# Optimization experiments

Hardware: AMD Instinct MI355X
Metric: run time of the kernel (lower is better)

The kernel has to match this reference:

```python
import jax, jax.numpy as jnp
import numpy as np

VOCAB, S, D, H, DH, L, W1S, DFF = 50265, 4096, 768, 12, 64, 2, 256, 3072


def layer_norm(x, g, b, eps=1e-5):
    m = jnp.mean(x, axis=-1, keepdims=True)
    v = jnp.mean((x - m) ** 2, axis=-1, keepdims=True)
    return (x - m) * jax.lax.rsqrt(v + eps) * g + b


def sliding_global_attn(q, k, v, att, w=W1S):
    # q,k,v: [B,H,S,Dh]; att: [B,S] float (1 real / 0 pad). Longformer-style
    # sliding window (one-sided w) + global attention on token 0.
    B, nh, S_, Dh = q.shape
    nc = S_ // w
    q = q * (Dh ** -0.5)
    k_pad = jnp.pad(k, ((0, 0), (0, 0), (w, w), (0, 0)))
    v_pad = jnp.pad(v, ((0, 0), (0, 0), (w, w), (0, 0)))
    idx = jnp.arange(nc)[:, None] * w + jnp.arange(3 * w)[None, :]  # [nc,3w] into padded axis
    k_band = k_pad[:, :, idx]  # [B,H,nc,3w,Dh]
    v_band = v_pad[:, :, idx]
    qc = q.reshape(B, nh, nc, w, Dh)
    s_loc = jnp.einsum('bhcqd,bhckd->bhcqk', qc, k_band)  # [B,H,nc,w,3w]
    rel = jnp.arange(3 * w)[None, :] - jnp.arange(w)[:, None]  # [w,3w]
    band_ok = (rel >= 0) & (rel <= 2 * w)
    key_abs = idx - w  # [nc,3w] absolute key positions
    in_seq = (key_abs >= 0) & (key_abs < S_) & (key_abs != 0)  # token 0 handled by global column
    key_real = att[:, jnp.clip(key_abs, 0, S_ - 1)] > 0  # [B,nc,3w]
    valid = band_ok[None, None, None] & in_seq[None, None, :, None, :] & key_real[:, None, :, None, :]
    s_loc = jnp.where(valid, s_loc, -1e9)
    s_g = jnp.einsum('bhcqd,bhd->bhcq', qc, k[:, :, 0])  # global key column
    p = jax.nn.softmax(jnp.concatenate([s_g[..., None], s_loc], axis=-1), axis=-1)
    out = (jnp.einsum('bhcq,bhd->bhcqd', p[..., 0], v[:, :, 0])
           + jnp.einsum('bhcqk,bhckd->bhcqd', p[..., 1:], v_band)).reshape(B, nh, S_, Dh)
    # global token 0 attends to everything
    s0 = jnp.where(att[:, None, :] > 0, jnp.einsum('bhd,bhsd->bhs', q[:, :, 0], k), -1e9)
    out0 = jnp.einsum('bhs,bhsd->bhd', jax.nn.softmax(s0, axis=-1), v)
    return out.at[:, :, 0].set(out0)


def setup_inputs() -> dict:
    key = jax.random.key(0)
    ks = jax.random.split(key, 16)
    sc = 0.02
    inp = {
        'input_ids': jax.random.randint(ks[0], (2, S), 0, VOCAB, dtype=jnp.int64)
        if jax.config.jax_enable_x64 else jax.random.randint(ks[0], (2, S), 0, VOCAB, dtype=jnp.int32),
        'attention_mask': jnp.ones((2, S), dtype=jnp.int32),
        'word_emb': sc * jax.random.normal(ks[1], (VOCAB, D), jnp.float32),
        'pos_emb': sc * jax.random.normal(ks[2], (S, D), jnp.float32),
        'emb_ln_g': jnp.ones((D,), jnp.float32), 'emb_ln_b': jnp.zeros((D,), jnp.float32),
        'Wq': sc * jax.random.normal(ks[3], (L, D, D), jnp.float32), 'bq': jnp.zeros((L, D), jnp.float32),
        'Wk': sc * jax.random.normal(ks[4], (L, D, D), jnp.float32), 'bk': jnp.zeros((L, D), jnp.float32),
        'Wv': sc * jax.random.normal(ks[5], (L, D, D), jnp.float32), 'bv': jnp.zeros((L, D), jnp.float32),
        'Wo': sc * jax.random.normal(ks[6], (L, D, D), jnp.float32), 'bo': jnp.zeros((L, D), jnp.float32),
        'ln1_g': jnp.ones((L, D), jnp.float32), 'ln1_b': jnp.zeros((L, D), jnp.float32),
        'Wf1': sc * jax.random.normal(ks[7], (L, D, DFF), jnp.float32), 'bf1': jnp.zeros((L, DFF), jnp.float32),
        'Wf2': sc * jax.random.normal(ks[8], (L, DFF, D), jnp.float32), 'bf2': jnp.zeros((L, D), jnp.float32),
        'ln2_g': jnp.ones((L, D), jnp.float32), 'ln2_b': jnp.zeros((L, D), jnp.float32),
        'Wh1': sc * jax.random.normal(ks[9], (D, 256), jnp.float32), 'bh1': jnp.zeros((256,), jnp.float32),
        'Wh2': sc * jax.random.normal(ks[10], (256, 14), jnp.float32), 'bh2': jnp.zeros((14,), jnp.float32),
    }
    return inp


def reference(input_ids, attention_mask, word_emb, pos_emb, emb_ln_g, emb_ln_b,
              Wq, bq, Wk, bk, Wv, bv, Wo, bo, ln1_g, ln1_b,
              Wf1, bf1, Wf2, bf2, ln2_g, ln2_b, Wh1, bh1, Wh2, bh2):
    B, S_ = input_ids.shape
    att = attention_mask.astype(jnp.float32)
    x = word_emb[input_ids] + pos_emb[None, :S_, :]
    x = layer_norm(x, emb_ln_g, emb_ln_b)
    for l in range(L):
        def heads(w, b):
            return (x @ w + b).reshape(B, S_, H, DH).transpose(0, 2, 1, 3)
        q = heads(Wq[l], bq[l]); k = heads(Wk[l], bk[l]); v = heads(Wv[l], bv[l])
        a = sliding_global_attn(q, k, v, att)
        a = a.transpose(0, 2, 1, 3).reshape(B, S_, D) @ Wo[l] + bo[l]
        x = layer_norm(x + a, ln1_g[l], ln1_b[l])
        f = jax.nn.gelu(x @ Wf1[l] + bf1[l]) @ Wf2[l] + bf2[l]
        x = layer_norm(x + f, ln2_g[l], ln2_b[l])
    # masked mean pool
    m = att[..., None]
    pooled = jnp.sum(x * m, axis=1) / jnp.clip(jnp.sum(m, axis=1), 1e-9)
    h = jax.nn.relu(pooled @ Wh1 + bh1)
    return jax.nn.sigmoid(h @ Wh2 + bh2) * 4.0
```

## Files before the change

kernel.cpp:

```cpp
#include <hip/hip_runtime.h>
#include <hip/hip_bf16.h>
#include <math.h>

#define S_LEN 4096
#define D_MODEL 768
#define NHEAD 12
#define DH 64
#define NLAYER 2
#define DFF 3072
#define BATCH 2
#define QSTR 2304

typedef __attribute__((ext_vector_type(8))) __bf16 bf16x8;
typedef __attribute__((ext_vector_type(4))) float f32x4;
typedef __attribute__((ext_vector_type(16))) float f32x16;

__device__ __forceinline__ unsigned short f2bf_bits(float f) {
  unsigned int u = __float_as_uint(f);
  unsigned int r = (u + 0x7fffu + ((u >> 16) & 1u)) >> 16;
  return (unsigned short)r;
}

__device__ __forceinline__ float bf2f(unsigned short u) {
  return __uint_as_float(((unsigned int)u) << 16);
}

__device__ __forceinline__ unsigned int cvtpk_bf16(float lo, float hi) {
  unsigned int d;
  asm("v_cvt_pk_bf16_f32 %0, %1, %2" : "=v"(d) : "v"(lo), "v"(hi));
  return d;
}

__device__ __forceinline__ float gelu_fast(float x) {
  float u = 0.7978845608028654f * (x + 0.044715f * x * x * x);
  float t2 = fminf(fmaxf(2.f * u, -18.f), 18.f);
  float e = __expf(t2);
  return 0.5f * x * (1.f + (e - 1.f) / (e + 1.f));
}

#define ASYNC_COPY16(gsrc, ldst)                                       \
  __builtin_amdgcn_global_load_lds(                                    \
      (const __attribute__((address_space(1))) void*)(gsrc),           \
      (__attribute__((address_space(3))) void*)(ldst), 16, 0, 0)

#define MFMA_BF16(a, b, c) __builtin_amdgcn_mfma_f32_16x16x32_bf16(a, b, c, 0, 0, 0)
#define MFMA32_BF16(a, b, c) __builtin_amdgcn_mfma_f32_32x32x16_bf16(a, b, c, 0, 0, 0)

__device__ __forceinline__ float blk_sum256(float v, float* lds) {
#pragma unroll
  for (int off = 32; off > 0; off >>= 1) v += __shfl_down(v, off, 64);
  __syncthreads();
  if ((threadIdx.x & 63) == 0) lds[threadIdx.x >> 6] = v;
  __syncthreads();
  return lds[0] + lds[1] + lds[2] + lds[3];
}

__global__ __launch_bounds__(256) void wconv_kernel(
    const float* __restrict__ Wq, const float* __restrict__ Wk,
    const float* __restrict__ Wv, const float* __restrict__ Wo,
    const float* __restrict__ Wf1, const float* __restrict__ Wf2,
    unsigned short* __restrict__ Wbf) {
  int id = blockIdx.x;
  const float* src;
  unsigned short* dst;
  int K, N, t;
  if (id < 4608) {
    int m = id / 576;
    t = id % 576;
    int layer = m >> 2, which = m & 3;
    const float* s = (which == 0) ? Wq : (which == 1) ? Wk : (which == 2) ? Wv : Wo;
    src = s + (size_t)layer * 589824;
    dst = Wbf + (size_t)layer * 7077888 + (size_t)which * 589824;
    K = 768; N = 768;
  } else if (id < 9216) {
    int j = id - 4608;
    int layer = j / 2304;
    t = j % 2304;
    src = Wf1 + (size_t)layer * 2359296;
    dst = Wbf + (size_t)layer * 7077888 + 2359296;
    K = 768; N = 3072;
  } else {
    int j = id - 9216;
    int layer = j / 2304;
    t = j % 2304;
    src = Wf2 + (size_t)layer * 2359296;
    dst = Wbf + (size_t)layer * 7077888 + 4718592;
    K = 3072; N = 768;
  }
  int tiles_n = N >> 5;
  int tk = t / tiles_n, tn = t % tiles_n;
  __shared__ float tile[32][33];
  int c = threadIdx.x & 31, r0 = threadIdx.x >> 5;
#pragma unroll
  for (int p = 0; p < 4; ++p) {
    int r = r0 + p * 8;
    tile[r][c] = src[(size_t)(tk * 32 + r) * N + tn * 32 + c];
  }
  __syncthreads();
#pragma unroll
  for (int p = 0; p < 4; ++p) {
    int r = r0 + p * 8;
    dst[(size_t)(tn * 32 + r) * K + tk * 32 + c] = f2bf_bits(tile[c][r]);
  }
}

__global__ __launch_bounds__(256) void embed_ln_kernel(
    const int* __restrict__ ids, const float* __restrict__ wemb,
    const float* __restrict__ pemb, const float* __restrict__ g,
    const float* __restrict__ b, unsigned short* __restrict__ Xb) {
  int row = blockIdx.x;
  int s = row % S_LEN;
  int id = ids[row];
  const float* we = wemb + (size_t)id * D_MODEL;
  const float* pe = pemb + (size_t)s * D_MODEL;
  int t = threadIdx.x;
  __shared__ float lds[4];
  float v0 = we[t] + pe[t];
  float v1 = we[t + 256] + pe[t + 256];
  float v2 = we[t + 512] + pe[t + 512];
  float mean = blk_sum256(v0 + v1 + v2, lds) * (1.f / 768.f);
  float d0 = v0 - mean, d1 = v1 - mean, d2 = v2 - mean;
  float var = blk_sum256(d0 * d0 + d1 * d1 + d2 * d2, lds) * (1.f / 768.f);
  float rs = rsqrtf(var + 1e-5f);
  unsigned short* xb = Xb + (size_t)row * D_MODEL;
  xb[t]       = f2bf_bits(d0 * rs * g[t] + b[t]);
  xb[t + 256] = f2bf_bits(d1 * rs * g[t + 256] + b[t + 256]);
  xb[t + 512] = f2bf_bits(d2 * rs * g[t + 512] + b[t + 512]);
}

__global__ __launch_bounds__(256) void ln_kernel(
    const float* __restrict__ T, const float* __restrict__ g,
    const float* __restrict__ b, unsigned short* __restrict__ Xb) {
  int row = blockIdx.x;
  const float* tp = T + (size_t)row * D_MODEL;
  int t = threadIdx.x;
  __shared__ float lds[4];
  float v0 = tp[t], v1 = tp[t + 256], v2 = tp[t + 512];
  float mean = blk_sum256(v0 + v1 + v2, lds) * (1.f / 768.f);
  float d0 = v0 - mean, d1 = v1 - mean, d2 = v2 - mean;
  float var = blk_sum256(d0 * d0 + d1 * d1 + d2 * d2, lds) * (1.f / 768.f);
  float rs = rsqrtf(var + 1e-5f);
  unsigned short* xb = Xb + (size_t)row * D_MODEL;
  xb[t]       = f2bf_bits(d0 * rs * g[t] + b[t]);
  xb[t + 256] = f2bf_bits(d1 * rs * g[t + 256] + b[t + 256]);
  xb[t + 512] = f2bf_bits(d2 * rs * g[t + 512] + b[t + 512]);
}

template <int MODE>
__global__ __launch_bounds__(256) void gemm32(
    const unsigned short* __restrict__ A, const unsigned short* __restrict__ Bt,
    const float* __restrict__ bias0, const float* __restrict__ bias1,
    const float* __restrict__ bias2, const unsigned short* __restrict__ ResBf,
    void* __restrict__ Cout, int M, int N, int K) {
  __shared__ unsigned short Abuf[3][128 * 32];
  __shared__ unsigned short Bbuf[3][128 * 32];
  const int tid = threadIdx.x;
  const int lane = tid & 63, w = tid >> 6;
  const int wm = w >> 1, wn = w & 1;
  const int l31 = lane & 31, l5 = lane >> 5;

  const int nbx = gridDim.x;
  const int nwg = nbx * gridDim.y;
  const int orig = blockIdx.y * nbx + blockIdx.x;
  const int wgid = (orig & 7) * (nwg >> 3) + (orig >> 3);
  const int m0 = (wgid / nbx) * 128, n0 = (wgid % nbx) * 128;

  f32x16 acc[2][2];
#pragma unroll
  for (int i = 0; i < 2; ++i)
#pragma unroll
    for (int j = 0; j < 2; ++j)
#pragma unroll
      for (int r = 0; r < 16; ++r) acc[i][j][r] = 0.f;

  const int s0 = w * 64 + lane, s1 = s0 + 256;
  const int r0 = s0 >> 2, c0 = (s0 & 3) ^ ((r0 >> 1) & 3);
  const int r1 = s1 >> 2, c1 = (s1 & 3) ^ ((r1 >> 1) & 3);
  const unsigned short* gA0 = A + (size_t)(m0 + r0) * K + c0 * 8;
  const unsigned short* gA1 = A + (size_t)(m0 + r1) * K + c1 * 8;
  const unsigned short* gB0 = Bt + (size_t)(n0 + r0) * K + c0 * 8;
  const unsigned short* gB1 = Bt + (size_t)(n0 + r1) * K + c1 * 8;
  const int dA0 = (w * 64) * 8, dA1 = (256 + w * 64) * 8;

  int aoff[2][2], boff[2][2];
#pragma unroll
  for (int mt = 0; mt < 2; ++mt) {
    int ra = wm * 64 + mt * 32 + l31;
    int rb = wn * 64 + mt * 32 + l31;
    int key_a = (ra >> 1) & 3, key_b = (rb >> 1) & 3;
#pragma unroll
    for (int ks = 0; ks < 2; ++ks) {
      aoff[mt][ks] = ra * 32 + ((((ks << 1) | l5) ^ key_a) << 3);
      boff[mt][ks] = rb * 32 + ((((ks << 1) | l5) ^ key_b) << 3);
    }
  }

#define STAGE(bsel)                                                       \
  {                                                                       \
    ASYNC_COPY16(gA0, &Abuf[bsel][dA0]);                                  \
    ASYNC_COPY16(gA1, &Abuf[bsel][dA1]);                                  \
    ASYNC_COPY16(gB0, &Bbuf[bsel][dA0]);                                  \
    ASYNC_COPY16(gB1, &Bbuf[bsel][dA1]);                                  \
    gA0 += 32; gA1 += 32; gB0 += 32; gB1 += 32;                           \
  }

  const int nk = K >> 5;
  STAGE(0);
  if (nk > 1) STAGE(1);
  asm volatile("s_waitcnt vmcnt(4)" ::: "memory");
  __builtin_amdgcn_s_barrier();
  __builtin_amdgcn_sched_barrier(0);

  int cur = 0;
  for (int kt = 0; kt < nk; ++kt) {
    if (kt + 2 < nk) {
      int nxt = cur + 2;
      if (nxt >= 3) nxt -= 3;
      STAGE(nxt);
    }
    bf16x8 av[2][2], bv[2][2];
#pragma unroll
    for (int mt = 0; mt < 2; ++mt)
#pragma unroll
      for (int ks = 0; ks < 2; ++ks) {
        av[mt][ks] = *(const bf16x8*)(&Abuf[cur][aoff[mt][ks]]);
        bv[mt][ks] = *(const bf16x8*)(&Bbuf[cur][boff[mt][ks]]);
      }
#pragma unroll
    for (int mt = 0; mt < 2; ++mt)
#pragma unroll
      for (int nt = 0; nt < 2; ++nt)
#pragma unroll
        for (int ks = 0; ks < 2; ++ks)
          acc[mt][nt] = MFMA32_BF16(av[mt][ks], bv[nt][ks], acc[mt][nt]);
    if (kt + 1 < nk) {
      if (kt + 2 < nk)
        asm volatile("s_waitcnt vmcnt(4)" ::: "memory");
      else
        asm volatile("s_waitcnt vmcnt(0)" ::: "memory");
      __builtin_amdgcn_s_barrier();
      __builtin_amdgcn_sched_barrier(0);
    }
    cur = (cur == 2) ? 0 : cur + 1;
  }
#undef STAGE

#pragma unroll
  for (int mt = 0; mt < 2; ++mt) {
#pragma unroll
    for (int nt = 0; nt < 2; ++nt) {
      int gc = n0 + wn * 64 + nt * 32 + l31;
      float bsv;
      if (MODE == 4)
        bsv = (gc < 768) ? bias0[gc] : (gc < 1536) ? bias1[gc - 768] : bias2[gc - 1536];
      else
        bsv = bias0[gc];
#pragma unroll
      for (int reg = 0; reg < 16; ++reg) {
        int gr = m0 + wm * 64 + mt * 32 + (reg & 3) + 8 * (reg >> 2) + 4 * l5;
        float v = acc[mt][nt][reg] + bsv;
        if (MODE == 1) v = gelu_fast(v);
        if (MODE == 4 && gc < 768) v *= 0.125f;
        if (MODE == 2) {
          v += bf2f(ResBf[(size_t)gr * 768 + gc]);
          ((float*)Cout)[(size_t)gr * N + gc] = v;
        } else {
          ((unsigned short*)Cout)[(size_t)gr * N + gc] = f2bf_bits(v);
        }
      }
    }
  }
}

__global__ __launch_bounds__(256) void vtrans_kernel(
    const unsigned short* __restrict__ Vsrc, unsigned short* __restrict__ Vt) {
  int kb = blockIdx.x, h = blockIdx.y, b = blockIdx.z;
  int k0 = kb * 64;
  const size_t bs = (size_t)b * S_LEN;
  const size_t bh = (size_t)(b * NHEAD + h);
  __shared__ unsigned short tile[64][72];
  int tid = threadIdx.x;
#pragma unroll
  for (int p = 0; p < 2; ++p) {
    int idx = p * 256 + tid;
    int key = idx >> 3, ch = idx & 7;
    bf16x8 v = *(const bf16x8*)(Vsrc + (bs + k0 + key) * QSTR + h * DH + ch * 8);
    *(bf16x8*)&tile[key][ch * 8] = v;
  }
  __syncthreads();
#pragma unroll
  for (int p = 0; p < 2; ++p) {
    int idx = p * 256 + tid;
    int d = idx >> 3, kc = idx & 7;
    unsigned int w0 = tile[kc * 8 + 0][d] | ((unsigned int)tile[kc * 8 + 1][d] << 16);
    unsigned int w1 = tile[kc * 8 + 2][d] | ((unsigned int)tile[kc * 8 + 3][d] << 16);
    unsigned int w2 = tile[kc * 8 + 4][d] | ((unsigned int)tile[kc * 8 + 5][d] << 16);
    unsigned int w3 = tile[kc * 8 + 6][d] | ((unsigned int)tile[kc * 8 + 7][d] << 16);
    uint4 out = make_uint4(w0, w1, w2, w3);
    *(uint4*)(Vt + (bh * 64 + d) * S_LEN + k0 + kc * 8) = out;
  }
}

__global__ __launch_bounds__(512) void band_attn_kernel(
    const unsigned short* __restrict__ Qg, const unsigned short* __restrict__ Kgb,
    const unsigned short* __restrict__ Vgb, const unsigned short* __restrict__ Vt,
    const int* __restrict__ att, unsigned short* __restrict__ Aout) {
  const int bid = blockIdx.x;
  const int tid = threadIdx.x;
  const int lane = tid & 63, wq = tid >> 6;
  const int g = lane >> 4, cl = lane & 15;

  __shared__ __align__(16) char smem[52224];

  if (bid >= 384) {
    int g2 = bid - 384;
    int h = g2 % NHEAD, b = g2 / NHEAD;
    const size_t bs = (size_t)b * S_LEN;
    float* sc = (float*)smem;
    float* q0 = sc + S_LEN;
    float* red = q0 + 64;
    float* part = red + 8;
    if (tid < 64) q0[tid] = bf2f(Qg[bs * QSTR + h * DH + tid]);
    __syncthreads();
    float lmax = -1e30f;
    for (int s = tid; s < S_LEN; s += 512) {
      const unsigned short* kp = Kgb + (bs + s) * QSTR + h * DH;
      float acc = 0.f;
#pragma unroll
      for (int cc = 0; cc < 8; ++cc) {
        uint4 u = *(const uint4*)(kp + cc * 8);
        const unsigned int* uu = (const unsigned int*)&u;
#pragma unroll
        for (int w2 = 0; w2 < 4; ++w2) {
          unsigned int x = uu[w2];
          acc += q0[cc * 8 + w2 * 2] * __uint_as_float(x << 16);
          acc += q0[cc * 8 + w2 * 2 + 1] * __uint_as_float(x & 0xffff0000u);
        }
      }
      acc = (att[b * S_LEN + s] > 0) ? acc : -1e9f;
      sc[s] = acc;
      lmax = fmaxf(lmax, acc);
    }
#pragma unroll
    for (int off = 32; off > 0; off >>= 1) lmax = fmaxf(lmax, __shfl_down(lmax, off, 64));
    __syncthreads();
    if (lane == 0) red[wq] = lmax;
    __syncthreads();
    float M = red[0];
#pragma unroll
    for (int i = 1; i < 8; ++i) M = fmaxf(M, red[i]);
    float lsum = 0.f;
    for (int s = tid; s < S_LEN; s += 512) {
      float p = __expf(sc[s] - M);
      sc[s] = p;
      lsum += p;
    }
#pragma unroll
    for (int off = 32; off > 0; off >>= 1) lsum += __shfl_down(lsum, off, 64);
    __syncthreads();
    if (lane == 0) red[wq] = lsum;
    __syncthreads();
    float L = red[0];
#pragma unroll
    for (int i = 1; i < 8; ++i) L += red[i];
    int d = tid & 63, chunk = tid >> 6;
    float acc2 = 0.f;
    for (int s = chunk * 512; s < (chunk + 1) * 512; ++s)
      acc2 += sc[s] * bf2f(Vgb[(bs + s) * QSTR + h * DH + d]);
    part[chunk * 64 + d] = acc2;
    __syncthreads();
    if (tid < 64) {
      float v = 0.f;
#pragma unroll
      for (int i = 0; i < 8; ++i) v += part[i * 64 + tid];
      Aout[bs * D_MODEL + h * DH + tid] = f2bf_bits(v / L);
    }
    return;
  }

  const int xcd = bid & 7, within = bid >> 3;
  const int flat = xcd * 48 + within;
  const int c = flat & 15;
  const int hb = flat >> 4;
  const int h = hb % NHEAD, b = hb / NHEAD;
  const size_t bs = (size_t)b * S_LEN;
  const size_t bh = (size_t)(b * NHEAD + h);

  unsigned short* Klds = (unsigned short*)smem;
  unsigned short* Vlds = Klds + 3 * 4096;
  float* kmaskAll = (float*)(Vlds + 3 * 4096);

  const int Q0 = c * 256;

  bf16x8 qf[2][2];
#pragma unroll
  for (int qt = 0; qt < 2; ++qt)
#pragma unroll
    for (int ks = 0; ks < 2; ++ks)
      qf[qt][ks] = *(const bf16x8*)(Qg + (bs + Q0 + wq * 32 + qt * 16 + cl) * QSTR +
                                    h * DH + ks * 32 + g * 8);

  float mrun[2], lrun[2];
  f32x4 oacc[2][4];
#pragma unroll
  for (int qt = 0; qt < 2; ++qt) {
    float sg = 0.f;
#pragma unroll
    for (int ks = 0; ks < 2; ++ks) {
      bf16x8 k0 = *(const bf16x8*)(Kgb + bs * QSTR + h * DH + ks * 32 + g * 8);
#pragma unroll
      for (int j = 0; j < 8; ++j) sg += (float)qf[qt][ks][j] * (float)k0[j];
    }
    sg += __shfl_xor(sg, 16, 64);
    sg += __shfl_xor(sg, 32, 64);
    mrun[qt] = sg;
    lrun[qt] = 1.f;
  }
#pragma unroll
  for (int dt = 0; dt < 4; ++dt) {
    float v0d = bf2f(Vgb[bs * QSTR + h * DH + dt * 16 + cl]);
    f32x4 vv = {v0d, v0d, v0d, v0d};
    oacc[0][dt] = vv;
    oacc[1][dt] = vv;
  }
  for (int i = tid; i < 768; i += 512) {
    int ka = Q0 - 256 + i;
    kmaskAll[i] = (ka >= 1 && ka < S_LEN && att[b * S_LEN + ka] > 0) ? 0.f : -1e9f;
  }
  __syncthreads();

  const int jlo = wq * 32, jhi = wq * 32 + 543;
  const int tlo = (Q0 < 256) ? 4 : 0;
  int thi = (S_LEN + 256 - Q0) >> 6;
  if (thi > 12) thi = 12;

  const int skey = tid >> 3, sch = tid & 7;
  const int srcswzK = (sch ^ (skey & 7)) * 8;

  auto STAGE_T = [&](int t) {
    int p = t % 3;
    int kb0 = Q0 - 256 + t * 64;
    const unsigned short* srcK = Kgb + (bs + kb0 + skey) * QSTR + h * DH + srcswzK;
    const unsigned short* srcV = Vt + (bh * 64 + skey) * S_LEN + kb0 + srcswzK;
    ASYNC_COPY16(srcK, Klds + p * 4096 + wq * 512);
    ASYNC_COPY16(srcV, Vlds + p * 4096 + wq * 512);
  };

  auto COMPUTE = [&](int t) {
    if (t * 64 + 63 < jlo || t * 64 > jhi) return;
    int p = t % 3;
    f32x4 accs[4][2];
#pragma unroll
    for (int kt = 0; kt < 4; ++kt) {
      accs[kt][0] = (f32x4){0.f, 0.f, 0.f, 0.f};
      accs[kt][1] = (f32x4){0.f, 0.f, 0.f, 0.f};
    }
#pragma unroll
    for (int ks = 0; ks < 2; ++ks) {
      bf16x8 kf[4];
#pragma unroll
      for (int kt = 0; kt < 4; ++kt) {
        int key = kt * 16 + cl;
        kf[kt] = *(const bf16x8*)(Klds + p * 4096 + key * 64 +
                                  (((ks * 4 + g) ^ (key & 7)) * 8));
      }
#pragma unroll
      for (int kt = 0; kt < 4; ++kt) {
        accs[kt][0] = MFMA_BF16(kf[kt], qf[0][ks], accs[kt][0]);
        accs[kt][1] = MFMA_BF16(kf[kt], qf[1][ks], accs[kt][1]);
      }
    }

#pragma unroll
    for (int qt = 0; qt < 2; ++qt) {
      int iq = wq * 32 + qt * 16 + cl;
      int relbase = t * 64 - iq;
      float pvv[4][4];
      float tmax = -1e30f;
#pragma unroll
      for (int kt = 0; kt < 4; ++kt)
#pragma unroll
        for (int r = 0; r < 4; ++r) {
          int key = kt * 16 + g * 4 + r;
          int rel = relbase + key;
          float x = accs[kt][qt][r] + kmaskAll[t * 64 + key];
          x = (rel >= 0 && rel <= 512) ? x : -1e9f;
          pvv[kt][r] = x;
          tmax = fmaxf(tmax, x);
        }
      tmax = fmaxf(tmax, __shfl_xor(tmax, 16, 64));
      tmax = fmaxf(tmax, __shfl_xor(tmax, 32, 64));
      float mnew = fmaxf(mrun[qt], tmax);
      float scale = __expf(mrun[qt] - mnew);
      mrun[qt] = mnew;
      float psum = 0.f;
#pragma unroll
      for (int kt = 0; kt < 4; ++kt)
#pragma unroll
        for (int r = 0; r < 4; ++r) {
          float pp = __expf(pvv[kt][r] - mnew);
          pvv[kt][r] = pp;
          psum += pp;
        }
      psum += __shfl_xor(psum, 16, 64);
      psum += __shfl_xor(psum, 32, 64);
      lrun[qt] = lrun[qt] * scale + psum;
      float scr[4];
#pragma unroll
      for (int r = 0; r < 4; ++r) scr[r] = __shfl(scale, g * 4 + r, 64);
#pragma unroll
      for (int dt = 0; dt < 4; ++dt) {
        oacc[qt][dt][0] *= scr[0];
        oacc[qt][dt][1] *= scr[1];
        oacc[qt][dt][2] *= scr[2];
        oacc[qt][dt][3] *= scr[3];
      }
#pragma unroll
      for (int ks = 0; ks < 2; ++ks) {
        unsigned int E0D0 = cvtpk_bf16(pvv[ks * 2][0], pvv[ks * 2][1]);
        unsigned int E0D1 = cvtpk_bf16(pvv[ks * 2][2], pvv[ks * 2][3]);
        unsigned int E1D0 = cvtpk_bf16(pvv[ks * 2 + 1][0], pvv[ks * 2 + 1][1]);
        unsigned int E1D1 = cvtpk_bf16(pvv[ks * 2 + 1][2], pvv[ks * 2 + 1][3]);
        int src0 = ((lane >> 4) & 1) * 32 + cl;
        int src1 = src0 + 16;
        unsigned int a0 = (unsigned int)__shfl((int)E0D0, src0, 64);
        unsigned int a1 = (unsigned int)__shfl((int)E0D1, src0, 64);
        unsigned int a2 = (unsigned int)__shfl((int)E0D0, src1, 64);
        unsigned int a3 = (unsigned int)__shfl((int)E0D1, src1, 64);
        unsigned int b0 = (unsigned int)__shfl((int)E1D0, src0, 64);
        unsigned int b1 = (unsigned int)__shfl((int)E1D1, src0, 64);
        unsigned int b2 = (unsigned int)__shfl((int)E1D0, src1, 64);
        unsigned int b3 = (unsigned int)__shfl((int)E1D1, src1, 64);
        bool hi = lane >= 32;
        union { unsigned int u[4]; bf16x8 v; } af;
        af.u[0] = hi ? b0 : a0;
        af.u[1] = hi ? b1 : a1;
        af.u[2] = hi ? b2 : a2;
        af.u[3] = hi ? b3 : a3;
#pragma unroll
        for (int dt = 0; dt < 4; ++dt) {
          int d = dt * 16 + cl;
          bf16x8 vf = *(const bf16x8*)(Vlds + p * 4096 + d * 64 +
                                       (((ks * 4 + g) ^ (d & 7)) * 8));
          oacc[qt][dt] = MFMA_BF16(af.v, vf, oacc[qt][dt]);
        }
      }
    }
  };

  STAGE_T(tlo);
  if (tlo + 1 < thi) STAGE_T(tlo + 1);
  for (int t = tlo; t < thi; ++t) {
    if (t + 1 < thi)
      asm volatile("s_waitcnt vmcnt(2)" ::: "memory");
    else
      asm volatile("s_waitcnt vmcnt(0)" ::: "memory");
    __builtin_amdgcn_s_barrier();
    __builtin_amdgcn_sched_barrier(0);
    if (t + 2 < thi) STAGE_T(t + 2);
    COMPUTE(t);
  }

#pragma unroll
  for (int qt = 0; qt < 2; ++qt) {
    float lr[4];
#pragma unroll
    for (int r = 0; r < 4; ++r) lr[r] = 1.f / __shfl(lrun[qt], g * 4 + r, 64);
#pragma unroll
    for (int dt = 0; dt < 4; ++dt)
#pragma unroll
      for (int r = 0; r < 4; ++r) {
        int row = Q0 + wq * 32 + qt * 16 + g * 4 + r;
        if (row != 0)
          Aout[(bs + row) * D_MODEL + h * DH + dt * 16 + cl] =
              f2bf_bits(oacc[qt][dt][r] * lr[r]);
      }
  }
}

__global__ __launch_bounds__(256) void pool1_kernel(
    const unsigned short* __restrict__ Xb, const int* __restrict__ att,
    float* __restrict__ ppart) {
  int sb = blockIdx.x, b = blockIdx.y, t = threadIdx.x;
  float a0 = 0.f, a1 = 0.f, a2 = 0.f;
  for (int s = sb * 256; s < sb * 256 + 256; ++s) {
    float a = (float)att[b * S_LEN + s];
    const unsigned short* xp = Xb + ((size_t)b * S_LEN + s) * D_MODEL;
    a0 += bf2f(xp[t]) * a; a1 += bf2f(xp[t + 256]) * a; a2 += bf2f(xp[t + 512]) * a;
  }
  float* pp = ppart + ((size_t)b * 16 + sb) * D_MODEL;
  pp[t] = a0; pp[t + 256] = a1; pp[t + 512] = a2;
}

__global__ __launch_bounds__(256) void pool2_kernel(
    const float* __restrict__ ppart, const int* __restrict__ att,
    float* __restrict__ pooled) {
  int b = blockIdx.x, t = threadIdx.x;
  float a0 = 0.f, a1 = 0.f, a2 = 0.f;
  for (int sb = 0; sb < 16; ++sb) {
    const float* pp = ppart + ((size_t)b * 16 + sb) * D_MODEL;
    a0 += pp[t]; a1 += pp[t + 256]; a2 += pp[t + 512];
  }
  float cnt = 0.f;
  for (int s = 0; s < S_LEN; ++s) cnt += (float)att[b * S_LEN + s];
  cnt = fmaxf(cnt, 1e-9f);
  pooled[b * D_MODEL + t]       = a0 / cnt;
  pooled[b * D_MODEL + t + 256] = a1 / cnt;
  pooled[b * D_MODEL + t + 512] = a2 / cnt;
}

__global__ __launch_bounds__(256) void head_kernel(
    const float* __restrict__ pooled, const float* __restrict__ Wh1,
    const float* __restrict__ bh1, const float* __restrict__ Wh2,
    const float* __restrict__ bh2, float* __restrict__ out) {
  __shared__ float hbuf[2][256];
  int t = threadIdx.x;
  for (int b = 0; b < 2; ++b) {
    float acc = bh1[t];
    for (int d = 0; d < D_MODEL; ++d) acc += pooled[b * D_MODEL + d] * Wh1[d * 256 + t];
    hbuf[b][t] = fmaxf(acc, 0.f);
  }
  __syncthreads();
  if (t < 28) {
    int b = t / 14, j = t % 14;
    float acc = bh2[j];
    for (int i = 0; i < 256; ++i) acc += hbuf[b][i] * Wh2[i * 14 + j];
    out[t] = 4.f / (1.f + __expf(-acc));
  }
}

extern "C" void kernel_launch(void* const* d_in, const int* in_sizes, int n_in,
                              void* d_out, int out_size, void* d_ws,
                              size_t ws_size, hipStream_t stream) {
  const int* ids    = (const int*)d_in[0];
  const int* att    = (const int*)d_in[1];
  const float* wemb = (const float*)d_in[2];
  const float* pemb = (const float*)d_in[3];
  const float* elng = (const float*)d_in[4];
  const float* elnb = (const float*)d_in[5];
  const float* Wq   = (const float*)d_in[6];
  const float* bq   = (const float*)d_in[7];
  const float* Wk   = (const float*)d_in[8];
  const float* bk   = (const float*)d_in[9];
  const float* Wv   = (const float*)d_in[10];
  const float* bv   = (const float*)d_in[11];
  const float* Wo   = (const float*)d_in[12];
  const float* bo   = (const float*)d_in[13];
  const float* ln1g = (const float*)d_in[14];
  const float* ln1b = (const float*)d_in[15];
  const float* Wf1  = (const float*)d_in[16];
  const float* bf1  = (const float*)d_in[17];
  const float* Wf2  = (const float*)d_in[18];
  const float* bf2  = (const float*)d_in[19];
  const float* ln2g = (const float*)d_in[20];
  const float* ln2b = (const float*)d_in[21];
  const float* Wh1  = (const float*)d_in[22];
  const float* bh1  = (const float*)d_in[23];
  const float* Wh2  = (const float*)d_in[24];
  const float* bh2  = (const float*)d_in[25];

  const int M = BATCH * S_LEN;
  float* ws = (float*)d_ws;
  float* T = ws;
  unsigned short* QKV  = (unsigned short*)(ws + 6291456);
  unsigned short* Vt   = (unsigned short*)(ws + 11010048);
  unsigned short* Abbf = (unsigned short*)(ws + 12582912);
  unsigned short* Xbf  = (unsigned short*)(ws + 15728640);
  unsigned short* FFbf = (unsigned short*)(ws + 18874368);
  unsigned short* Wbf  = (unsigned short*)(ws + 31457280);
  float* pooled = ws + 38535168;
  float* ppart  = ws + 38536704;

  wconv_kernel<<<13824, 256, 0, stream>>>(Wq, Wk, Wv, Wo, Wf1, Wf2, Wbf);
  embed_ln_kernel<<<M, 256, 0, stream>>>(ids, wemb, pemb, elng, elnb, Xbf);

  for (int l = 0; l < NLAYER; ++l) {
    const unsigned short* wqkv = Wbf + (size_t)l * 7077888;
    const unsigned short* wot  = wqkv + 1769472;
    const unsigned short* wf1t = wqkv + 2359296;
    const unsigned short* wf2t = wqkv + 4718592;

    gemm32<4><<<dim3(18, 64), 256, 0, stream>>>(
        Xbf, wqkv, bq + l * D_MODEL, bk + l * D_MODEL, bv + l * D_MODEL,
        nullptr, QKV, M, QSTR, 768);

    vtrans_kernel<<<dim3(64, NHEAD, BATCH), 256, 0, stream>>>(QKV + 1536, Vt);
    band_attn_kernel<<<408, 512, 0, stream>>>(
        QKV, QKV + 768, QKV + 1536, Vt, att, Abbf);

    gemm32<2><<<dim3(6, 64), 256, 0, stream>>>(
        Abbf, wot, bo + l * D_MODEL, nullptr, nullptr, Xbf, T, M, 768, 768);
    ln_kernel<<<M, 256, 0, stream>>>(T, ln1g + l * D_MODEL, ln1b + l * D_MODEL, Xbf);

    gemm32<1><<<dim3(24, 64), 256, 0, stream>>>(
        Xbf, wf1t, bf1 + l * DFF, nullptr, nullptr, nullptr, FFbf, M, DFF, 768);
    gemm32<2><<<dim3(6, 64), 256, 0, stream>>>(
        FFbf, wf2t, bf2 + l * D_MODEL, nullptr, nullptr, Xbf, T, M, 768, DFF);
    ln_kernel<<<M, 256, 0, stream>>>(T, ln2g + l * D_MODEL, ln2b + l * D_MODEL, Xbf);
  }

  pool1_kernel<<<dim3(16, BATCH), 256, 0, stream>>>(Xbf, att, ppart);
  pool2_kernel<<<BATCH, 256, 0, stream>>>(ppart, att, pooled);
  head_kernel<<<1, 256, 0, stream>>>(pooled, Wh1, bh1, Wh2, bh2, (float*)d_out);
}
```

Baseline: 831.3 us.

## Drop LDS staging in band attention; read K/V directly from global memory

The banded attention kernel no longer stages K and V tiles into LDS through a triple-buffered async-copy pipeline with barriers. Each wave now loads its MFMA fragments directly from global memory (K rows and transposed V), relying on L2/cache reuse across waves. The key padding mask is precomputed once per forward by a new small kernel, so the kernel no longer builds a per-block LDS mask. This removes barriers and LDS traffic and shrinks shared memory, but it duplicates global loads across the 8 waves and loses the latency hiding the prefetch pipeline provided.

```diff
diff --git a/kernel.cpp b/kernel.cpp
--- a/kernel.cpp
+++ b/kernel.cpp
@@ -104,6 +104,13 @@
   }
 }
 
+__global__ __launch_bounds__(256) void mask_kernel(
+    const int* __restrict__ att, float* __restrict__ maskF) {
+  int i = blockIdx.x * 256 + threadIdx.x;
+  int b = i >> 12, ka = i & 4095;
+  maskF[i] = (ka >= 1 && att[b * S_LEN + ka] > 0) ? 0.f : -1e9f;
+}
+
 __global__ __launch_bounds__(256) void embed_ln_kernel(
     const int* __restrict__ ids, const float* __restrict__ wemb,
     const float* __restrict__ pemb, const float* __restrict__ g,
@@ -304,19 +311,20 @@
 __global__ __launch_bounds__(512) void band_attn_kernel(
     const unsigned short* __restrict__ Qg, const unsigned short* __restrict__ Kgb,
     const unsigned short* __restrict__ Vgb, const unsigned short* __restrict__ Vt,
-    const int* __restrict__ att, unsigned short* __restrict__ Aout) {
+    const int* __restrict__ att, const float* __restrict__ maskF,
+    unsigned short* __restrict__ Aout) {
   const int bid = blockIdx.x;
   const int tid = threadIdx.x;
   const int lane = tid & 63, wq = tid >> 6;
   const int g = lane >> 4, cl = lane & 15;
 
-  __shared__ __align__(16) char smem[52224];
+  __shared__ __align__(16) float smemg[4680];
 
   if (bid >= 384) {
     int g2 = bid - 384;
     int h = g2 % NHEAD, b = g2 / NHEAD;
     const size_t bs = (size_t)b * S_LEN;
-    float* sc = (float*)smem;
+    float* sc = smemg;
     float* q0 = sc + S_LEN;
     float* red = q0 + 64;
     float* part = red + 8;
@@ -385,11 +393,6 @@
   const int h = hb % NHEAD, b = hb / NHEAD;
   const size_t bs = (size_t)b * S_LEN;
   const size_t bh = (size_t)(b * NHEAD + h);
-
-  unsigned short* Klds = (unsigned short*)smem;
-  unsigned short* Vlds = Klds + 3 * 4096;
-  float* kmaskAll = (float*)(Vlds + 3 * 4096);
-
   const int Q0 = c * 256;
 
   bf16x8 qf[2][2];
@@ -423,32 +426,16 @@
     oacc[0][dt] = vv;
     oacc[1][dt] = vv;
   }
-  for (int i = tid; i < 768; i += 512) {
-    int ka = Q0 - 256 + i;
-    kmaskAll[i] = (ka >= 1 && ka < S_LEN && att[b * S_LEN + ka] > 0) ? 0.f : -1e9f;
-  }
-  __syncthreads();
 
   const int jlo = wq * 32, jhi = wq * 32 + 543;
   const int tlo = (Q0 < 256) ? 4 : 0;
   int thi = (S_LEN + 256 - Q0) >> 6;
   if (thi > 12) thi = 12;
 
-  const int skey = tid >> 3, sch = tid & 7;
-  const int srcswzK = (sch ^ (skey & 7)) * 8;
-
-  auto STAGE_T = [&](int t) {
-    int p = t % 3;
-    int kb0 = Q0 - 256 + t * 64;
-    const unsigned short* srcK = Kgb + (bs + kb0 + skey) * QSTR + h * DH + srcswzK;
-    const unsigned short* srcV = Vt + (bh * 64 + skey) * S_LEN + kb0 + srcswzK;
-    ASYNC_COPY16(srcK, Klds + p * 4096 + wq * 512);
-    ASYNC_COPY16(srcV, Vlds + p * 4096 + wq * 512);
-  };
-
-  auto COMPUTE = [&](int t) {
-    if (t * 64 + 63 < jlo || t * 64 > jhi) return;
-    int p = t % 3;
+  for (int t = tlo; t < thi; ++t) {
+    if (t * 64 + 63 < jlo || t * 64 > jhi) continue;
+    const int kabs0 = Q0 - 256 + t * 64;
+
     f32x4 accs[4][2];
 #pragma unroll
     for (int kt = 0; kt < 4; ++kt) {
@@ -459,17 +446,20 @@
     for (int ks = 0; ks < 2; ++ks) {
       bf16x8 kf[4];
 #pragma unroll
-      for (int kt = 0; kt < 4; ++kt) {
-        int key = kt * 16 + cl;
-        kf[kt] = *(const bf16x8*)(Klds + p * 4096 + key * 64 +
-                                  (((ks * 4 + g) ^ (key & 7)) * 8));
-      }
+      for (int kt = 0; kt < 4; ++kt)
+        kf[kt] = *(const bf16x8*)(Kgb + (bs + kabs0 + kt * 16 + cl) * QSTR +
+                                  h * DH + ks * 32 + g * 8);
 #pragma unroll
       for (int kt = 0; kt < 4; ++kt) {
         accs[kt][0] = MFMA_BF16(kf[kt], qf[0][ks], accs[kt][0]);
         accs[kt][1] = MFMA_BF16(kf[kt], qf[1][ks], accs[kt][1]);
       }
     }
+
+    float4 mk[4];
+#pragma unroll
+    for (int kt = 0; kt < 4; ++kt)
+      mk[kt] = *(const float4*)(maskF + b * S_LEN + kabs0 + kt * 16 + g * 4);
 
 #pragma unroll
     for (int qt = 0; qt < 2; ++qt) {
@@ -478,16 +468,18 @@
       float pvv[4][4];
       float tmax = -1e30f;
 #pragma unroll
-      for (int kt = 0; kt < 4; ++kt)
+      for (int kt = 0; kt < 4; ++kt) {
+        const float* mkf = (const float*)&mk[kt];
 #pragma unroll
         for (int r = 0; r < 4; ++r) {
           int key = kt * 16 + g * 4 + r;
           int rel = relbase + key;
-          float x = accs[kt][qt][r] + kmaskAll[t * 64 + key];
+          float x = accs[kt][qt][r] + mkf[r];
           x = (rel >= 0 && rel <= 512) ? x : -1e9f;
           pvv[kt][r] = x;
           tmax = fmaxf(tmax, x);
         }
+      }
       tmax = fmaxf(tmax, __shfl_xor(tmax, 16, 64));
       tmax = fmaxf(tmax, __shfl_xor(tmax, 32, 64));
       float mnew = fmaxf(mrun[qt], tmax);
@@ -539,26 +531,12 @@
         af.u[3] = hi ? b3 : a3;
 #pragma unroll
         for (int dt = 0; dt < 4; ++dt) {
-          int d = dt * 16 + cl;
-          bf16x8 vf = *(const bf16x8*)(Vlds + p * 4096 + d * 64 +
-                                       (((ks * 4 + g) ^ (d & 7)) * 8));
+          bf16x8 vf = *(const bf16x8*)(Vt + (bh * 64 + dt * 16 + cl) * S_LEN +
+                                       kabs0 + (ks * 4 + g) * 8);
           oacc[qt][dt] = MFMA_BF16(af.v, vf, oacc[qt][dt]);
         }
       }
     }
-  };
-
-  STAGE_T(tlo);
-  if (tlo + 1 < thi) STAGE_T(tlo + 1);
-  for (int t = tlo; t < thi; ++t) {
-    if (t + 1 < thi)
-      asm volatile("s_waitcnt vmcnt(2)" ::: "memory");
-    else
-      asm volatile("s_waitcnt vmcnt(0)" ::: "memory");
-    __builtin_amdgcn_s_barrier();
-    __builtin_amdgcn_sched_barrier(0);
-    if (t + 2 < thi) STAGE_T(t + 2);
-    COMPUTE(t);
   }
 
 #pragma unroll
@@ -670,8 +648,10 @@
   unsigned short* Wbf  = (unsigned short*)(ws + 31457280);
   float* pooled = ws + 38535168;
   float* ppart  = ws + 38536704;
+  float* maskF  = ws + 38561280;
 
   wconv_kernel<<<13824, 256, 0, stream>>>(Wq, Wk, Wv, Wo, Wf1, Wf2, Wbf);
+  mask_kernel<<<32, 256, 0, stream>>>(att, maskF);
   embed_ln_kernel<<<M, 256, 0, stream>>>(ids, wemb, pemb, elng, elnb, Xbf);
 
   for (int l = 0; l < NLAYER; ++l) {
@@ -686,7 +666,7 @@
 
     vtrans_kernel<<<dim3(64, NHEAD, BATCH), 256, 0, stream>>>(QKV + 1536, Vt);
     band_attn_kernel<<<408, 512, 0, stream>>>(
-        QKV, QKV + 768, QKV + 1536, Vt, att, Abbf);
+        QKV, QKV + 768, QKV + 1536, Vt, att, maskF, Abbf);
 
     gemm32<2><<<dim3(6, 64), 256, 0, stream>>>(
         Abbf, wot, bo + l * D_MODEL, nullptr, nullptr, Xbf, T, M, 768, 768);
```

Measured after the change: 851.1 us. +2.4%, slower.
